# Performance work log

Measured on AMD Instinct MI355X. Metric: run time of the kernel, lower is better.

Reference implementation:

```python
import jax, jax.numpy as jnp
import numpy as np

EPS = 1e-6

def _layernorm(x, gamma, beta):
    mu = jnp.mean(x, axis=-1, keepdims=True)
    var = jnp.mean(jnp.square(x - mu), axis=-1, keepdims=True)
    return (x - mu) * jax.lax.rsqrt(var + EPS) * gamma + beta


def setup_inputs() -> dict:
    key = jax.random.key(0)
    ks = jax.random.split(key, 8)
    B, N, C, F = 2, 2048, 1024, 4096
    s = 0.02
    return {
        "x": jax.random.normal(ks[0], (B, N, C), jnp.float32),
        "Wq": jax.random.normal(ks[1], (C, C), jnp.float32) * s,
        "Wk": jax.random.normal(ks[2], (C, C), jnp.float32) * s,
        "Wv": jax.random.normal(ks[3], (C, C), jnp.float32) * s,
        "Wp": jax.random.normal(ks[4], (C, C), jnp.float32) * s,
        "bp": jnp.zeros((C,), jnp.float32),
        "W1": jax.random.normal(ks[5], (C, F), jnp.float32) * s,
        "b1": jnp.zeros((F,), jnp.float32),
        "W2": jax.random.normal(ks[6], (F, C), jnp.float32) * s,
        "b2": jnp.zeros((C,), jnp.float32),
        "gamma1": jnp.ones((C,), jnp.float32),
        "beta1": jnp.zeros((C,), jnp.float32),
        "gamma2": jnp.ones((C,), jnp.float32),
        "beta2": jnp.zeros((C,), jnp.float32),
    }


def reference(x, Wq, Wk, Wv, Wp, bp, W1, b1, W2, b2, gamma1, beta1, gamma2, beta2):
    B, N, C = x.shape
    H = 16
    D = C // H
    scale = D ** -0.5

    xn = _layernorm(x, gamma1, beta1)
    # QKV projections (no bias); q pre-scaled by head_dim**-0.5 as in source
    q = (xn @ Wq * scale).reshape(B, N, H, D).transpose(0, 2, 1, 3)  # bhnd
    k = (xn @ Wk).reshape(B, N, H, D).transpose(0, 2, 1, 3)
    v = (xn @ Wv).reshape(B, N, H, D).transpose(0, 2, 1, 3)

    attn = jax.nn.softmax(jnp.einsum("bhnd,bhmd->bhnm", q, k), axis=-1)
    y = jnp.einsum("bhnm,bhmd->bhnd", attn, v)
    y = y.transpose(0, 2, 1, 3).reshape(B, N, C)
    x = x + (y @ Wp + bp)

    xn2 = _layernorm(x, gamma2, beta2)
    h = jax.nn.gelu(xn2 @ W1 + b1, approximate=False)  # keras 'gelu' is exact
    x = x + (h @ W2 + b2)
    return x
```

## Files before the change

### kernel.cpp

```cpp
#include <hip/hip_runtime.h>
#include <math.h>

#define BN  4096
#define SEQ 2048
#define CH  1024
#define FF  4096
#define NH  16
#define HD  64

typedef short bf16x8 __attribute__((ext_vector_type(8)));
typedef float f32x4  __attribute__((ext_vector_type(4)));

#define MFMA16(a,b,c) __builtin_amdgcn_mfma_f32_16x16x32_bf16(a,b,c,0,0,0)

__device__ __forceinline__ unsigned short f2b(float f){
  unsigned u = __float_as_uint(f);
  u += 0x7fffu + ((u>>16)&1u);
  return (unsigned short)(u>>16);
}

__device__ __forceinline__ unsigned pk2(float a, float b){
  return __builtin_amdgcn_perm(__float_as_uint(b), __float_as_uint(a), 0x07060302u);
}

#if __has_builtin(__builtin_amdgcn_exp2f)
__device__ __forceinline__ float fexp2(float x){ return __builtin_amdgcn_exp2f(x); }
#else
__device__ __forceinline__ float fexp2(float x){
  float r; asm("v_exp_f32 %0, %1" : "=v"(r) : "v"(x)); return r;
}
#endif

__device__ __forceinline__ void gl2lds16(const void* g, void* l){
  __builtin_amdgcn_global_load_lds(
      (__attribute__((address_space(1))) void*)g,
      (__attribute__((address_space(3))) void*)l, 16, 0, 0);
}

__global__ __launch_bounds__(256) void transpose_cvt(const float* __restrict__ in,
    unsigned short* __restrict__ out, int R, int S, float scale)
{
  __shared__ float tile[64][65];
  const int tid = threadIdx.x;
  const int tx = tid & 63, ty = tid >> 6;
  const int s0 = blockIdx.x * 64, r0 = blockIdx.y * 64;
  #pragma unroll
  for (int j = 0; j < 16; j++){
    int r = ty + j*4;
    tile[r][tx] = in[(size_t)(r0 + r)*S + s0 + tx];
  }
  __syncthreads();
  #pragma unroll
  for (int j = 0; j < 16; j++){
    int s = ty + j*4;
    out[(size_t)(s0 + s)*R + r0 + tx] = f2b(tile[tx][s] * scale);
  }
}

__global__ __launch_bounds__(256) void ln_kernel(const float* __restrict__ x,
    const float* __restrict__ gamma, const float* __restrict__ beta,
    unsigned short* __restrict__ out)
{
  const int row = blockIdx.x, tid = threadIdx.x;
  const float4 xv = ((const float4*)(x + (size_t)row*CH))[tid];
  float s  = xv.x + xv.y + xv.z + xv.w;
  float ss = xv.x*xv.x + xv.y*xv.y + xv.z*xv.z + xv.w*xv.w;
  #pragma unroll
  for (int off = 1; off < 64; off <<= 1){
    s  += __shfl_xor(s,  off, 64);
    ss += __shfl_xor(ss, off, 64);
  }
  __shared__ float red[8];
  const int w = tid >> 6;
  if ((tid & 63) == 0){ red[w] = s; red[4+w] = ss; }
  __syncthreads();
  s  = red[0]+red[1]+red[2]+red[3];
  ss = red[4]+red[5]+red[6]+red[7];
  const float mu   = s * (1.f/CH);
  const float rstd = rsqrtf(ss*(1.f/CH) - mu*mu + 1e-6f);
  const float4 g = ((const float4*)gamma)[tid];
  const float4 b = ((const float4*)beta )[tid];
  ushort4 o;
  o.x = f2b((xv.x-mu)*rstd*g.x + b.x);
  o.y = f2b((xv.y-mu)*rstd*g.y + b.y);
  o.z = f2b((xv.z-mu)*rstd*g.z + b.z);
  o.w = f2b((xv.w-mu)*rstd*g.w + b.w);
  ((ushort4*)(out + (size_t)row*CH))[tid] = o;
}

template<int BNT,int BIAS,int GELU,int RES,int OMODE>
__global__ __launch_bounds__(256,2) void gemm_bt(const unsigned short* __restrict__ A,
    const unsigned short* __restrict__ Bt, const float* __restrict__ bias,
    const float* __restrict__ resid, float* __restrict__ outF,
    unsigned short* __restrict__ outB, unsigned short* __restrict__ outK,
    unsigned short* __restrict__ outV, int M, int Nn, int K)
{
  constexpr int MI = (BNT==128) ? 4 : 2;
  __shared__ __align__(16) unsigned short Al[128*32];
  __shared__ __align__(16) unsigned short Bl[BNT*32];
  const int tid = threadIdx.x;
  const int w = tid >> 6, lane = tid & 63;
  const int quad = lane >> 4, l16 = lane & 15;
  const int m0 = blockIdx.y*128, n0 = blockIdx.x*BNT;
  const int wm = (BNT==128) ? (w >> 1)*64 : w*32;
  const int wn = (BNT==128) ? (w & 1)*64 : 0;
  const int srow = lane >> 2, scol = (lane & 3)*8;
  f32x4 acc[MI][4] = {};
  for (int k0 = 0; k0 < K; k0 += 32){
    __syncthreads();
    #pragma unroll
    for (int i = 0; i < 2; i++){
      const int roff = (i*4 + w)*16;
      gl2lds16(A + (size_t)(m0 + roff + srow)*K + k0 + scol, (char*)Al + roff*64);
      if (BNT == 128)
        gl2lds16(Bt + (size_t)(n0 + roff + srow)*K + k0 + scol, (char*)Bl + roff*64);
    }
    if (BNT == 64){
      const int roff = w*16;
      gl2lds16(Bt + (size_t)(n0 + roff + srow)*K + k0 + scol, (char*)Bl + roff*64);
    }
    __syncthreads();
    bf16x8 af[MI], bfr[4];
    #pragma unroll
    for (int mi = 0; mi < MI; mi++)
      af[mi] = *(const bf16x8*)(Al + (wm + mi*16 + l16)*32 + quad*8);
    #pragma unroll
    for (int nj = 0; nj < 4; nj++)
      bfr[nj] = *(const bf16x8*)(Bl + (wn + nj*16 + l16)*32 + quad*8);
    #pragma unroll
    for (int mi = 0; mi < MI; mi++)
      #pragma unroll
      for (int nj = 0; nj < 4; nj++)
        acc[mi][nj] = MFMA16(af[mi], bfr[nj], acc[mi][nj]);
  }
  #pragma unroll
  for (int nj = 0; nj < 4; nj++){
    const int col = n0 + wn + nj*16 + l16;
    const float bv = BIAS ? bias[col] : 0.f;
    #pragma unroll
    for (int mi = 0; mi < MI; mi++){
      #pragma unroll
      for (int r = 0; r < 4; r++){
        const int row = m0 + wm + mi*16 + quad*4 + r;
        float v = acc[mi][nj][r] + bv;
        if (GELU) v = 0.5f*v*(1.f + erff(v*0.70710678118654752f));
        if (RES)  v += resid[(size_t)row*Nn + col];
        if (OMODE == 0) outF[(size_t)row*Nn + col] = v;
        else if (OMODE == 1) outB[(size_t)row*Nn + col] = f2b(v);
        else if (OMODE == 2){
          const int bb = row >> 11, n = row & (SEQ-1);
          const int hh = col >> 6,  d = col & (HD-1);
          const int np = (n & ~63) | (((n & 15) << 2) | ((n >> 4) & 3));
          outB[((size_t)((bb*NH + hh)*HD + d))*SEQ + np] = f2b(v);
        } else {
          const int cg = col >> 10, c = col & (CH-1);
          if (cg == 0)      outB[(size_t)row*CH + c] = f2b(v);
          else if (cg == 1) outK[(size_t)row*CH + c] = f2b(v);
          else {
            const int bb = row >> 11, n = row & (SEQ-1);
            const int hh = c >> 6,  d = c & (HD-1);
            const int np = (n & ~63) | (((n & 15) << 2) | ((n >> 4) & 3));
            outV[((size_t)((bb*NH + hh)*HD + d))*SEQ + np] = f2b(v);
          }
        }
      }
    }
  }
}

__global__ __launch_bounds__(256,2) void attn_kernel(const unsigned short* __restrict__ q,
    const unsigned short* __restrict__ k, const unsigned short* __restrict__ vt,
    unsigned short* __restrict__ y)
{
  __shared__ __align__(16) unsigned short Kl[2][64*64];
  __shared__ __align__(16) unsigned short Vl[2][64*64];
  __shared__ __align__(16) unsigned short Pp[4][64*68];
  const int tid = threadIdx.x;
  const int w = tid >> 6, lane = tid & 63;
  const int wq = w & 1, wk = w >> 1;
  const int quad = lane >> 4, l16 = lane & 15;
  const int bh = blockIdx.y;
  const int b = bh >> 4, h = bh & 15;
  const size_t tb  = ((size_t)b*SEQ)*CH + h*HD;
  const size_t vb_ = (size_t)bh*HD*SEQ;
  const int qr0 = blockIdx.x*128 + wq*64;

  bf16x8 qf[4][2];
  #pragma unroll
  for (int mi = 0; mi < 4; mi++)
    #pragma unroll
    for (int kc = 0; kc < 2; kc++)
      qf[mi][kc] = *(const bf16x8*)(q + tb + (size_t)(qr0 + mi*16 + l16)*CH + kc*32 + quad*8);

  float sacc[4][4];
  f32x4 o[4][4] = {};
  #pragma unroll
  for (int mi = 0; mi < 4; mi++)
    #pragma unroll
    for (int r = 0; r < 4; r++) sacc[mi][r] = 0.f;

  for (int t = 0; t < 16; t++){
    const int kv0 = wk*1024 + t*64;
    __syncthreads();
    #pragma unroll
    for (int i = 0; i < 8; i++){
      const int r = i*8 + (lane >> 3);
      const int c = (lane & 7) ^ (r & 7);
      if (wq == 0)
        gl2lds16(k  + tb  + (size_t)(kv0 + r)*CH + c*8, (char*)&Kl[wk][0] + i*1024);
      else
        gl2lds16(vt + vb_ + (size_t)r*SEQ + kv0 + c*8, (char*)&Vl[wk][0] + i*1024);
    }
    __syncthreads();

    f32x4 s[4][4] = {};
    #pragma unroll
    for (int kc = 0; kc < 2; kc++){
      #pragma unroll
      for (int nj = 0; nj < 4; nj++){
        bf16x8 kf = *(const bf16x8*)(&Kl[wk][0] + (nj*16 + l16)*64 + (((kc*4 + quad) ^ (l16 & 7))*8));
        #pragma unroll
        for (int mi = 0; mi < 4; mi++)
          s[mi][nj] = MFMA16(qf[mi][kc], kf, s[mi][nj]);
      }
    }
    #pragma unroll
    for (int mi = 0; mi < 4; mi++){
      #pragma unroll
      for (int r = 0; r < 4; r++){
        const float p0 = fexp2(s[mi][0][r]);
        const float p1 = fexp2(s[mi][1][r]);
        const float p2 = fexp2(s[mi][2][r]);
        const float p3 = fexp2(s[mi][3][r]);
        sacc[mi][r] += (p0 + p1) + (p2 + p3);
        uint2 pk;
        pk.x = pk2(p0, p1);
        pk.y = pk2(p2, p3);
        const int prow = mi*16 + quad*4 + r;
        *(uint2*)(&Pp[w][prow*68 + l16*4]) = pk;
      }
    }
    #pragma unroll
    for (int kc = 0; kc < 2; kc++){
      bf16x8 pa[4];
      #pragma unroll
      for (int mi = 0; mi < 4; mi++)
        pa[mi] = *(const bf16x8*)(&Pp[w][(mi*16 + l16)*68 + kc*32 + quad*8]);
      #pragma unroll
      for (int nd = 0; nd < 4; nd++){
        bf16x8 vf = *(const bf16x8*)(&Vl[wk][0] + (nd*16 + l16)*64 + (((kc*4 + quad) ^ (l16 & 7))*8));
        #pragma unroll
        for (int mi = 0; mi < 4; mi++)
          o[mi][nd] = MFMA16(pa[mi], vf, o[mi][nd]);
      }
    }
  }

  __syncthreads();
  float* ob = wq ? (float*)&Vl[0][0] : (float*)&Kl[0][0];
  float* sb = (float*)&Pp[2 + wq][0];
  if (wk == 1){
    #pragma unroll
    for (int mi = 0; mi < 4; mi++)
      #pragma unroll
      for (int nd = 0; nd < 4; nd++)
        #pragma unroll
        for (int r = 0; r < 4; r++){
          const int idx = (mi*4 + nd)*4 + r;
          ob[lane*64 + ((idx + lane) & 63)] = o[mi][nd][r];
        }
    #pragma unroll
    for (int mi = 0; mi < 4; mi++)
      #pragma unroll
      for (int r = 0; r < 4; r++)
        sb[lane*16 + ((mi*4 + r + lane) & 15)] = sacc[mi][r];
  }
  __syncthreads();
  if (wk == 0){
    #pragma unroll
    for (int mi = 0; mi < 4; mi++)
      #pragma unroll
      for (int nd = 0; nd < 4; nd++)
        #pragma unroll
        for (int r = 0; r < 4; r++){
          const int idx = (mi*4 + nd)*4 + r;
          o[mi][nd][r] += ob[lane*64 + ((idx + lane) & 63)];
        }
    #pragma unroll
    for (int mi = 0; mi < 4; mi++){
      #pragma unroll
      for (int r = 0; r < 4; r++){
        float sum = sacc[mi][r] + sb[lane*16 + ((mi*4 + r + lane) & 15)];
        #pragma unroll
        for (int off = 1; off < 16; off <<= 1) sum += __shfl_xor(sum, off, 64);
        const float inv = 1.f / sum;
        const int qr = qr0 + mi*16 + quad*4 + r;
        #pragma unroll
        for (int nd = 0; nd < 4; nd++)
          y[tb + (size_t)qr*CH + nd*16 + l16] = f2b(o[mi][nd][r]*inv);
      }
    }
  }
}

extern "C" void kernel_launch(void* const* d_in, const int* in_sizes, int n_in,
                              void* d_out, int out_size, void* d_ws, size_t ws_size,
                              hipStream_t stream)
{
  (void)in_sizes; (void)n_in; (void)out_size; (void)ws_size;
  const float* x   = (const float*)d_in[0];
  const float* Wq  = (const float*)d_in[1];
  const float* Wk  = (const float*)d_in[2];
  const float* Wv  = (const float*)d_in[3];
  const float* Wp  = (const float*)d_in[4];
  const float* bp  = (const float*)d_in[5];
  const float* W1  = (const float*)d_in[6];
  const float* b1  = (const float*)d_in[7];
  const float* W2  = (const float*)d_in[8];
  const float* b2  = (const float*)d_in[9];
  const float* g1  = (const float*)d_in[10];
  const float* be1 = (const float*)d_in[11];
  const float* g2  = (const float*)d_in[12];
  const float* be2 = (const float*)d_in[13];
  float* out = (float*)d_out;
  char* ws = (char*)d_ws;
  const size_t MB = 1024*1024;
  unsigned short* wq_t = (unsigned short*)(ws +  0*MB);
  unsigned short* wk_t = (unsigned short*)(ws +  2*MB);
  unsigned short* wv_t = (unsigned short*)(ws +  4*MB);
  unsigned short* wp_t = (unsigned short*)(ws +  6*MB);
  unsigned short* w1_t = (unsigned short*)(ws +  8*MB);
  unsigned short* w2_t = (unsigned short*)(ws + 16*MB);
  unsigned short* xn   = (unsigned short*)(ws + 24*MB);
  unsigned short* qb   = (unsigned short*)(ws + 32*MB);
  unsigned short* kb   = (unsigned short*)(ws + 40*MB);
  unsigned short* vtb  = (unsigned short*)(ws + 48*MB);
  unsigned short* yb   = (unsigned short*)(ws + 56*MB);
  float*          x2   = (float*)         (ws + 64*MB);
  unsigned short* xn2  = (unsigned short*)(ws + 80*MB);
  unsigned short* hb   = (unsigned short*)(ws + 88*MB);

  transpose_cvt<<<dim3(16,16),256,0,stream>>>(Wq, wq_t, CH, CH, 0.18033688011112042f);
  transpose_cvt<<<dim3(16,16),256,0,stream>>>(Wk, wk_t, CH, CH, 1.f);
  transpose_cvt<<<dim3(16,16),256,0,stream>>>(Wv, wv_t, CH, CH, 1.f);
  transpose_cvt<<<dim3(16,16),256,0,stream>>>(Wp, wp_t, CH, CH, 1.f);
  transpose_cvt<<<dim3(64,16),256,0,stream>>>(W1, w1_t, CH, FF, 1.f);
  transpose_cvt<<<dim3(16,64),256,0,stream>>>(W2, w2_t, FF, CH, 1.f);

  ln_kernel<<<BN,256,0,stream>>>(x, g1, be1, xn);
  gemm_bt<128,0,0,0,3><<<dim3(24,32),256,0,stream>>>(xn, wq_t, nullptr, nullptr,
      nullptr, qb, kb, vtb, BN, 3072, CH);
  attn_kernel<<<dim3(16,32),256,0,stream>>>(qb, kb, vtb, yb);
  gemm_bt<64,1,0,1,0><<<dim3(16,32),256,0,stream>>>(yb, wp_t, bp, x, x2,
      nullptr, nullptr, nullptr, BN, CH, CH);
  ln_kernel<<<BN,256,0,stream>>>(x2, g2, be2, xn2);
  gemm_bt<128,1,1,0,1><<<dim3(32,32),256,0,stream>>>(xn2, w1_t, b1, nullptr, nullptr,
      hb, nullptr, nullptr, BN, FF, CH);
  gemm_bt<64,1,0,1,0><<<dim3(16,32),256,0,stream>>>(hb, w2_t, b2, x2, out,
      nullptr, nullptr, nullptr, BN, CH, FF);
}
```

Baseline: 395.9 us.

## Double GEMM K-tile with XOR-swizzled LDS and split-K for FFN down-projection

Result: faster. 373.4 us (-5.7%).

```diff
diff --git a/kernel.cpp b/kernel.cpp
--- a/kernel.cpp
+++ b/kernel.cpp
@@ -88,7 +88,7 @@
   ((ushort4*)(out + (size_t)row*CH))[tid] = o;
 }
 
-template<int BNT,int BIAS,int GELU,int RES,int OMODE>
+template<int BNT,int BIAS,int GELU,int RES,int OMODE,int SPLITK>
 __global__ __launch_bounds__(256,2) void gemm_bt(const unsigned short* __restrict__ A,
     const unsigned short* __restrict__ Bt, const float* __restrict__ bias,
     const float* __restrict__ resid, float* __restrict__ outF,
@@ -96,42 +96,55 @@
     unsigned short* __restrict__ outV, int M, int Nn, int K)
 {
   constexpr int MI = (BNT==128) ? 4 : 2;
-  __shared__ __align__(16) unsigned short Al[128*32];
-  __shared__ __align__(16) unsigned short Bl[BNT*32];
+  constexpr int BCH = (BNT==128) ? 4 : 2;
+  __shared__ __align__(16) unsigned short Al[128*64];
+  __shared__ __align__(16) unsigned short Bl[BNT*64];
   const int tid = threadIdx.x;
   const int w = tid >> 6, lane = tid & 63;
   const int quad = lane >> 4, l16 = lane & 15;
   const int m0 = blockIdx.y*128, n0 = blockIdx.x*BNT;
   const int wm = (BNT==128) ? (w >> 1)*64 : w*32;
   const int wn = (BNT==128) ? (w & 1)*64 : 0;
-  const int srow = lane >> 2, scol = (lane & 3)*8;
+  const int srow = lane >> 3, sslot = lane & 7;
   f32x4 acc[MI][4] = {};
-  for (int k0 = 0; k0 < K; k0 += 32){
+  const int kseg = SPLITK > 1 ? K / SPLITK : K;
+  const int kBeg = SPLITK > 1 ? blockIdx.z * kseg : 0;
+  for (int k0 = kBeg; k0 < kBeg + kseg; k0 += 64){
     __syncthreads();
     #pragma unroll
-    for (int i = 0; i < 2; i++){
-      const int roff = (i*4 + w)*16;
-      gl2lds16(A + (size_t)(m0 + roff + srow)*K + k0 + scol, (char*)Al + roff*64);
-      if (BNT == 128)
-        gl2lds16(Bt + (size_t)(n0 + roff + srow)*K + k0 + scol, (char*)Bl + roff*64);
-    }
-    if (BNT == 64){
-      const int roff = w*16;
-      gl2lds16(Bt + (size_t)(n0 + roff + srow)*K + k0 + scol, (char*)Bl + roff*64);
+    for (int i = 0; i < 4; i++){
+      const int rb = (w*4 + i)*8;
+      const int r = rb + srow;
+      const int c = sslot ^ (r & 7);
+      gl2lds16(A + (size_t)(m0 + r)*K + k0 + c*8, (char*)Al + rb*128);
+    }
+    #pragma unroll
+    for (int i = 0; i < BCH; i++){
+      const int rb = (w*BCH + i)*8;
+      const int r = rb + srow;
+      const int c = sslot ^ (r & 7);
+      gl2lds16(Bt + (size_t)(n0 + r)*K + k0 + c*8, (char*)Bl + rb*128);
     }
     __syncthreads();
-    bf16x8 af[MI], bfr[4];
-    #pragma unroll
-    for (int mi = 0; mi < MI; mi++)
-      af[mi] = *(const bf16x8*)(Al + (wm + mi*16 + l16)*32 + quad*8);
-    #pragma unroll
-    for (int nj = 0; nj < 4; nj++)
-      bfr[nj] = *(const bf16x8*)(Bl + (wn + nj*16 + l16)*32 + quad*8);
-    #pragma unroll
-    for (int mi = 0; mi < MI; mi++)
-      #pragma unroll
-      for (int nj = 0; nj < 4; nj++)
-        acc[mi][nj] = MFMA16(af[mi], bfr[nj], acc[mi][nj]);
+    #pragma unroll
+    for (int kc = 0; kc < 2; kc++){
+      bf16x8 af[MI], bfr[4];
+      #pragma unroll
+      for (int mi = 0; mi < MI; mi++){
+        const int r = wm + mi*16 + l16;
+        af[mi] = *(const bf16x8*)(Al + r*64 + (((kc*4 + quad) ^ (r & 7))*8));
+      }
+      #pragma unroll
+      for (int nj = 0; nj < 4; nj++){
+        const int r = wn + nj*16 + l16;
+        bfr[nj] = *(const bf16x8*)(Bl + r*64 + (((kc*4 + quad) ^ (r & 7))*8));
+      }
+      #pragma unroll
+      for (int mi = 0; mi < MI; mi++)
+        #pragma unroll
+        for (int nj = 0; nj < 4; nj++)
+          acc[mi][nj] = MFMA16(af[mi], bfr[nj], acc[mi][nj]);
+    }
   }
   #pragma unroll
   for (int nj = 0; nj < 4; nj++){
@@ -142,17 +155,21 @@
       #pragma unroll
       for (int r = 0; r < 4; r++){
         const int row = m0 + wm + mi*16 + quad*4 + r;
-        float v = acc[mi][nj][r] + bv;
+        float v = acc[mi][nj][r];
+        if (SPLITK > 1){
+          if (blockIdx.z == 0){
+            if (BIAS) v += bias[col];
+            if (RES)  v += resid[(size_t)row*Nn + col];
+          }
+          atomicAdd(&outF[(size_t)row*Nn + col], v);
+          continue;
+        }
+        v += bv;
         if (GELU) v = 0.5f*v*(1.f + erff(v*0.70710678118654752f));
         if (RES)  v += resid[(size_t)row*Nn + col];
         if (OMODE == 0) outF[(size_t)row*Nn + col] = v;
         else if (OMODE == 1) outB[(size_t)row*Nn + col] = f2b(v);
-        else if (OMODE == 2){
-          const int bb = row >> 11, n = row & (SEQ-1);
-          const int hh = col >> 6,  d = col & (HD-1);
-          const int np = (n & ~63) | (((n & 15) << 2) | ((n >> 4) & 3));
-          outB[((size_t)((bb*NH + hh)*HD + d))*SEQ + np] = f2b(v);
-        } else {
+        else {
           const int cg = col >> 10, c = col & (CH-1);
           if (cg == 0)      outB[(size_t)row*CH + c] = f2b(v);
           else if (cg == 1) outK[(size_t)row*CH + c] = f2b(v);
@@ -348,14 +365,15 @@
   transpose_cvt<<<dim3(16,64),256,0,stream>>>(W2, w2_t, FF, CH, 1.f);
 
   ln_kernel<<<BN,256,0,stream>>>(x, g1, be1, xn);
-  gemm_bt<128,0,0,0,3><<<dim3(24,32),256,0,stream>>>(xn, wq_t, nullptr, nullptr,
+  gemm_bt<128,0,0,0,3,0><<<dim3(24,32),256,0,stream>>>(xn, wq_t, nullptr, nullptr,
       nullptr, qb, kb, vtb, BN, 3072, CH);
   attn_kernel<<<dim3(16,32),256,0,stream>>>(qb, kb, vtb, yb);
-  gemm_bt<64,1,0,1,0><<<dim3(16,32),256,0,stream>>>(yb, wp_t, bp, x, x2,
+  gemm_bt<64,1,0,1,0,0><<<dim3(16,32),256,0,stream>>>(yb, wp_t, bp, x, x2,
       nullptr, nullptr, nullptr, BN, CH, CH);
   ln_kernel<<<BN,256,0,stream>>>(x2, g2, be2, xn2);
-  gemm_bt<128,1,1,0,1><<<dim3(32,32),256,0,stream>>>(xn2, w1_t, b1, nullptr, nullptr,
+  gemm_bt<128,1,1,0,1,0><<<dim3(32,32),256,0,stream>>>(xn2, w1_t, b1, nullptr, nullptr,
       hb, nullptr, nullptr, BN, FF, CH);
-  gemm_bt<64,1,0,1,0><<<dim3(16,32),256,0,stream>>>(hb, w2_t, b2, x2, out,
+  hipMemsetAsync(out, 0, (size_t)BN*CH*sizeof(float), stream);
+  gemm_bt<64,1,0,1,0,2><<<dim3(16,32,2),256,0,stream>>>(hb, w2_t, b2, x2, out,
       nullptr, nullptr, nullptr, BN, CH, FF);
 }
```
